# Performance work log

Hardware: AMD Instinct MI355X
Metric: run time of the kernel (lower is better)

The kernel has to match this reference:

```python
import jax, jax.numpy as jnp
import numpy as np

B, S, D, H = 2, 48, 256, 8
DH = D // H  # depth per head = 32
N = S * S    # flattened pair sequence length = 2304


def setup_inputs() -> dict:
    key = jax.random.key(0)
    ks = jax.random.split(key, 9)
    std = 1.0 / np.sqrt(D)
    x = jax.random.normal(ks[0], (B, S, S, D), dtype=jnp.float32)
    Wq = jax.random.normal(ks[1], (D, D), dtype=jnp.float32) * std
    Wk = jax.random.normal(ks[2], (D, D), dtype=jnp.float32) * std
    Wv = jax.random.normal(ks[3], (D, D), dtype=jnp.float32) * std
    Wo = jax.random.normal(ks[4], (D, D), dtype=jnp.float32) * std
    bq = jnp.zeros((D,), jnp.float32)
    bk = jnp.zeros((D,), jnp.float32)
    bv = jnp.zeros((D,), jnp.float32)
    bo = jnp.zeros((D,), jnp.float32)
    return {"pair_representation": x, "Wq": Wq, "bq": bq, "Wk": Wk, "bk": bk,
            "Wv": Wv, "bv": bv, "Wo": Wo, "bo": bo}


def reference(pair_representation, Wq, bq, Wk, bk, Wv, bv, Wo, bo):
    x = pair_representation.reshape(B, N, D)  # flatten (S,S) -> N

    def heads(t):  # (B,N,D) -> (B,H,N,DH)
        return t.reshape(B, N, H, DH).transpose(0, 2, 1, 3)

    q = heads(x @ Wq + bq)
    k = heads(x @ Wk + bk)
    v = heads(x @ Wv + bv)

    scale = 1.0 / jnp.sqrt(jnp.asarray(DH, jnp.float32))
    logits = jnp.einsum('bhnd,bhmd->bhnm', q, k) * scale  # (B,H,N,N)
    attn = jax.nn.softmax(logits, axis=-1)
    ctx = jnp.einsum('bhnm,bhmd->bhnd', attn, v)
    ctx = ctx.transpose(0, 2, 1, 3).reshape(B, N, D)
    return ctx @ Wo + bo  # (B, N, D)
```

## Files before the change

### kernel.cpp

```cpp
#include <hip/hip_runtime.h>
#include <math.h>

#define B 2
#define S 48
#define D 256
#define H 8
#define DH 32
#define N (S*S)
#define BN (B*N)
#define BH (B*H)
#define KS 6
#define KPZ (N/KS)
#define NE ((size_t)BN*D)
#define BHN (BH*N)

typedef _Float16 half8 __attribute__((ext_vector_type(8)));
typedef _Float16 half4_t __attribute__((ext_vector_type(4)));
typedef unsigned short ushort8_t __attribute__((ext_vector_type(8)));
typedef float floatx4 __attribute__((ext_vector_type(4)));

__device__ __forceinline__ half8 cvt8(const float* v) {
    half8 h;
    #pragma unroll
    for (int j = 0; j < 8; j++) h[j] = (_Float16)v[j];
    return h;
}

__global__ __launch_bounds__(256) void proj_kernel(
    const float* __restrict__ x,
    const float* __restrict__ Wq, const float* __restrict__ bq,
    const float* __restrict__ Wk, const float* __restrict__ bk,
    const float* __restrict__ Wv, const float* __restrict__ bv,
    _Float16* __restrict__ qbuf, _Float16* __restrict__ kbuf,
    _Float16* __restrict__ vtbuf)
{
    __shared__ __align__(16) _Float16 BhS[128 * 72];

    const int z = blockIdx.z;
    const float* W    = (z == 0) ? Wq : (z == 1) ? Wk : Wv;
    const float* bias = (z == 0) ? bq : (z == 1) ? bk : bv;
    const float scale = (z == 0) ? rsqrtf((float)DH) * 1.44269504f : 1.0f;

    const int t = threadIdx.x;
    const int wv2 = t >> 6, lane = t & 63, l15 = lane & 15, quad = lane >> 4;
    const int rowb = blockIdx.x * 64;
    const int colb = blockIdx.y * 128;
    const int grow = rowb + wv2 * 16 + l15;
    floatx4 acc[8] = {{0,0,0,0},{0,0,0,0},{0,0,0,0},{0,0,0,0},
                      {0,0,0,0},{0,0,0,0},{0,0,0,0},{0,0,0,0}};

    for (int kb0 = 0; kb0 < D; kb0 += 64) {
        __syncthreads();
        #pragma unroll
        for (int i = 0; i < 4; i++) {
            int u = i * 256 + t;
            int cc = u & 127, k0 = (u >> 7) * 8;
            float v[8];
            #pragma unroll
            for (int j = 0; j < 8; j++)
                v[j] = W[(size_t)(kb0 + k0 + j) * D + colb + cc];
            *(half8*)(BhS + cc * 72 + k0) = cvt8(v);
        }
        __syncthreads();
        #pragma unroll
        for (int ksx = 0; ksx < 2; ksx++) {
            const float* xp = x + (size_t)grow * D + kb0 + ksx * 32 + quad * 8;
            float4 x0 = *(const float4*)xp;
            float4 x1 = *(const float4*)(xp + 4);
            float v[8] = {x0.x, x0.y, x0.z, x0.w, x1.x, x1.y, x1.z, x1.w};
            half8 ah = cvt8(v);
            #pragma unroll
            for (int cg = 0; cg < 8; cg++) {
                half8 bh8 = *(const half8*)(BhS + (cg * 16 + l15) * 72 + ksx * 32 + quad * 8);
                acc[cg] = __builtin_amdgcn_mfma_f32_16x16x32_f16(ah, bh8, acc[cg], 0, 0, 0);
            }
        }
    }

    const int bb = (rowb >= N) ? 1 : 0;
    #pragma unroll
    for (int cg = 0; cg < 8; cg++) {
        int col = colb + cg * 16 + l15;
        int hh = col >> 5, dh = col & 31;
        float bs = bias[col];
        if (z < 2) {
            _Float16* op = (z == 0) ? qbuf : kbuf;
            #pragma unroll
            for (int r = 0; r < 4; r++) {
                int n = rowb + wv2 * 16 + quad * 4 + r - bb * N;
                float v = (acc[cg][r] + bs) * scale;
                op[((size_t)(bb * H + hh) * N + n) * DH + dh] = (_Float16)v;
            }
        } else {
            int n0 = rowb + wv2 * 16 + quad * 4 - bb * N;
            half4_t pk;
            #pragma unroll
            for (int r = 0; r < 4; r++) pk[r] = (_Float16)(acc[cg][r] + bs);
            *(half4_t*)(vtbuf + ((size_t)(bb * H + hh) * DH + dh) * N + n0) = pk;
        }
    }
}

__global__ __launch_bounds__(256) void attn_kernel(
    const _Float16* __restrict__ qbuf, const _Float16* __restrict__ kbuf,
    const _Float16* __restrict__ vtbuf,
    _Float16* __restrict__ ctx_part, float* __restrict__ lpart)
{
    __shared__ __align__(16) _Float16 Ks[128 * 40];
    __shared__ __align__(16) _Float16 Vt[32 * 136];

    const int t = threadIdx.x;
    const int wv2 = t >> 6, lane = t & 63, l15 = lane & 15, quad = lane >> 4;
    const int bh = blockIdx.y, kz = blockIdx.z;
    const int qbase = blockIdx.x * 128 + wv2 * 32;

    half8 bq8[2];
    #pragma unroll
    for (int qg = 0; qg < 2; qg++)
        bq8[qg] = *(const half8*)(qbuf +
            ((size_t)bh * N + qbase + qg * 16 + l15) * DH + quad * 8);

    floatx4 acc[2][2] = {{{0,0,0,0},{0,0,0,0}},{{0,0,0,0},{0,0,0,0}}};
    float lsum[2] = {0.f, 0.f};

    for (int it = 0; it < KPZ / 128; it++) {
        const int key0 = kz * KPZ + it * 128;
        __syncthreads();
        #pragma unroll
        for (int i = 0; i < 2; i++) {
            int u = i * 256 + t;
            *(ushort8_t*)(Ks + (u >> 2) * 40 + (u & 3) * 8) =
                *(const ushort8_t*)(kbuf + ((size_t)bh * N + key0 + (u >> 2)) * DH + (u & 3) * 8);
            *(ushort8_t*)(Vt + (u >> 4) * 136 + (u & 15) * 8) =
                *(const ushort8_t*)(vtbuf + ((size_t)bh * DH + (u >> 4)) * N + key0 + (u & 15) * 8);
        }
        __syncthreads();

        #pragma unroll
        for (int kg = 0; kg < 8; kg++) {
            half8 ka = *(const half8*)(Ks + (kg * 16 + l15) * 40 + quad * 8);
            half4_t va0 = *(const half4_t*)(Vt + l15 * 136 + kg * 16 + quad * 4);
            half4_t va1 = *(const half4_t*)(Vt + (16 + l15) * 136 + kg * 16 + quad * 4);
            #pragma unroll
            for (int qg = 0; qg < 2; qg++) {
                floatx4 s = {0, 0, 0, 0};
                s = __builtin_amdgcn_mfma_f32_16x16x32_f16(ka, bq8[qg], s, 0, 0, 0);
                half4_t pf;
                #pragma unroll
                for (int r = 0; r < 4; r++) {
                    float p = exp2f(s[r]);
                    lsum[qg] += p;
                    pf[r] = (_Float16)p;
                }
                acc[qg][0] = __builtin_amdgcn_mfma_f32_16x16x16f16(va0, pf, acc[qg][0], 0, 0, 0);
                acc[qg][1] = __builtin_amdgcn_mfma_f32_16x16x16f16(va1, pf, acc[qg][1], 0, 0, 0);
            }
        }
    }

    const int bb = bh >> 3, hh = bh & 7;
    #pragma unroll
    for (int qg = 0; qg < 2; qg++) {
        float ls = lsum[qg];
        ls += __shfl_xor(ls, 16);
        ls += __shfl_xor(ls, 32);
        int q = qbase + qg * 16 + l15;
        if (quad == 0) lpart[(size_t)kz * BHN + bh * N + q] = ls;
        _Float16* crow = ctx_part + (size_t)kz * NE + ((size_t)bb * N + q) * D + hh * DH;
        half4_t c0, c1;
        #pragma unroll
        for (int r = 0; r < 4; r++) {
            c0[r] = (_Float16)acc[qg][0][r];
            c1[r] = (_Float16)acc[qg][1][r];
        }
        *(half4_t*)(crow + quad * 4)      = c0;
        *(half4_t*)(crow + 16 + quad * 4) = c1;
    }
}

__global__ __launch_bounds__(256) void outproj_kernel(
    const _Float16* __restrict__ ctx_part, const float* __restrict__ lpart,
    const float* __restrict__ Wo, const float* __restrict__ bo,
    float* __restrict__ out)
{
    __shared__ __align__(16) _Float16 BhS[128 * 72];
    __shared__ __align__(16) _Float16 AsS[32 * 72];
    __shared__ float Linv[32 * 8];

    const int t = threadIdx.x;
    const int wv2 = t >> 6, lane = t & 63, l15 = lane & 15, quad = lane >> 4;
    const int wr = wv2 >> 1, wc = wv2 & 1;
    const int rowb = blockIdx.x * 32;
    const int colb = blockIdx.y * 128;

    {
        int r = t >> 3, hh = t & 7;
        int row = rowb + r;
        int bb = (row >= N) ? 1 : 0;
        int bhn = (bb * H + hh) * N + (row - bb * N);
        float ls = 0.f;
        #pragma unroll
        for (int zz = 0; zz < KS; zz++) ls += lpart[(size_t)zz * BHN + bhn];
        Linv[t] = 1.0f / ls;
    }

    floatx4 acc[4] = {{0,0,0,0},{0,0,0,0},{0,0,0,0},{0,0,0,0}};

    for (int kb0 = 0; kb0 < D; kb0 += 64) {
        __syncthreads();
        {
            int r = t >> 3, k0 = (t & 7) * 8;
            int row = rowb + r;
            int kcol = kb0 + k0;
            float linv = Linv[r * 8 + (kcol >> 5)];
            float v[8] = {};
            #pragma unroll
            for (int zz = 0; zz < KS; zz++) {
                half8 h = *(const half8*)(ctx_part + (size_t)zz * NE + (size_t)row * D + kcol);
                #pragma unroll
                for (int j = 0; j < 8; j++) v[j] += (float)h[j];
            }
            #pragma unroll
            for (int j = 0; j < 8; j++) v[j] *= linv;
            *(half8*)(AsS + r * 72 + k0) = cvt8(v);
        }
        #pragma unroll
        for (int i = 0; i < 4; i++) {
            int u = i * 256 + t;
            int cc = u & 127, k0 = (u >> 7) * 8;
            float v[8];
            #pragma unroll
            for (int j = 0; j < 8; j++)
                v[j] = Wo[(size_t)(kb0 + k0 + j) * D + colb + cc];
            *(half8*)(BhS + cc * 72 + k0) = cvt8(v);
        }
        __syncthreads();
        #pragma unroll
        for (int ksx = 0; ksx < 2; ksx++) {
            half8 ah = *(const half8*)(AsS + (wr * 16 + l15) * 72 + ksx * 32 + quad * 8);
            #pragma unroll
            for (int cg = 0; cg < 4; cg++) {
                half8 bh8 = *(const half8*)(BhS + (wc * 64 + cg * 16 + l15) * 72 + ksx * 32 + quad * 8);
                acc[cg] = __builtin_amdgcn_mfma_f32_16x16x32_f16(ah, bh8, acc[cg], 0, 0, 0);
            }
        }
    }

    #pragma unroll
    for (int cg = 0; cg < 4; cg++) {
        int col = colb + wc * 64 + cg * 16 + l15;
        float bs = bo[col];
        #pragma unroll
        for (int r = 0; r < 4; r++) {
            int row = rowb + wr * 16 + quad * 4 + r;
            out[(size_t)row * D + col] = acc[cg][r] + bs;
        }
    }
}

extern "C" void kernel_launch(void* const* d_in, const int* in_sizes, int n_in,
                              void* d_out, int out_size, void* d_ws, size_t ws_size,
                              hipStream_t stream)
{
    const float* x  = (const float*)d_in[0];
    const float* Wq = (const float*)d_in[1];
    const float* bq = (const float*)d_in[2];
    const float* Wk = (const float*)d_in[3];
    const float* bk = (const float*)d_in[4];
    const float* Wv = (const float*)d_in[5];
    const float* bv = (const float*)d_in[6];
    const float* Wo = (const float*)d_in[7];
    const float* bo = (const float*)d_in[8];
    float* out = (float*)d_out;

    _Float16* ctx_part = (_Float16*)d_ws;
    float* lpart    = (float*)(ctx_part + (size_t)KS * NE);
    _Float16* qbuf  = (_Float16*)(lpart + (size_t)KS * BHN);
    _Float16* kbuf  = qbuf + NE;
    _Float16* vtbuf = kbuf + NE;

    proj_kernel<<<dim3(BN / 64, D / 128, 3), 256, 0, stream>>>(
        x, Wq, bq, Wk, bk, Wv, bv, qbuf, kbuf, vtbuf);

    attn_kernel<<<dim3(N / 128, BH, KS), 256, 0, stream>>>(
        qbuf, kbuf, vtbuf, ctx_part, lpart);

    outproj_kernel<<<dim3(BN / 32, D / 128), 256, 0, stream>>>(
        ctx_part, lpart, Wo, bo, out);
}
```

Measured before the change: 132.0 us.

## Pre-convert x and weights to fp16 in a prep kernel; restructure outproj tiling

Adds a prep kernel that converts x to fp16 and transposes all four weight matrices into fp16 column-major once. The projection and output kernels then load fp16 data with vector loads instead of doing strided fp32 gathers and conversions. The output projection reads Wo straight from global memory with smaller 16-row tiles. The attention kernel packs probabilities with cvt_pkrtz and stores the partial row sums in a per-row layout so outproj can read them contiguously. The cost is an extra launch plus an extra write and read of x in fp16.

Result: no change. 132.3 us (+0.2%).

```diff
diff --git a/kernel.cpp b/kernel.cpp
--- a/kernel.cpp
+++ b/kernel.cpp
@@ -16,6 +16,7 @@
 
 typedef _Float16 half8 __attribute__((ext_vector_type(8)));
 typedef _Float16 half4_t __attribute__((ext_vector_type(4)));
+typedef __fp16 fp16x2 __attribute__((ext_vector_type(2)));
 typedef unsigned short ushort8_t __attribute__((ext_vector_type(8)));
 typedef float floatx4 __attribute__((ext_vector_type(4)));
 
@@ -26,18 +27,57 @@
     return h;
 }
 
+__global__ __launch_bounds__(256) void prep_kernel(
+    const float* __restrict__ x,
+    const float* __restrict__ Wq, const float* __restrict__ Wk,
+    const float* __restrict__ Wv, const float* __restrict__ Wo,
+    _Float16* __restrict__ xh, _Float16* __restrict__ Wt)
+{
+    __shared__ __align__(16) _Float16 Ls[64 * 72];
+    const int t = threadIdx.x;
+    const int bid = blockIdx.x;
+    if (bid < 64) {
+        const int z = bid >> 4, tile = bid & 15;
+        const int k0 = (tile >> 2) * 64, c0 = (tile & 3) * 64;
+        const float* W = (z == 0) ? Wq : (z == 1) ? Wk : (z == 2) ? Wv : Wo;
+        #pragma unroll
+        for (int r = 0; r < 4; r++) {
+            int k = r * 16 + (t >> 4);
+            int c = (t & 15) * 4;
+            float4 f = *(const float4*)(W + (size_t)(k0 + k) * D + c0 + c);
+            Ls[(c + 0) * 72 + k] = (_Float16)f.x;
+            Ls[(c + 1) * 72 + k] = (_Float16)f.y;
+            Ls[(c + 2) * 72 + k] = (_Float16)f.z;
+            Ls[(c + 3) * 72 + k] = (_Float16)f.w;
+        }
+        __syncthreads();
+        #pragma unroll
+        for (int i = 0; i < 2; i++) {
+            int u = i * 256 + t;
+            int c = u >> 3, ko = (u & 7) * 8;
+            *(ushort8_t*)(Wt + (size_t)(z * D + c0 + c) * D + k0 + ko) =
+                *(const ushort8_t*)(Ls + c * 72 + ko);
+        }
+    } else {
+        size_t g = ((size_t)(bid - 64) * 256 + t) * 8;
+        float4 f0 = *(const float4*)(x + g);
+        float4 f1 = *(const float4*)(x + g + 4);
+        float v[8] = {f0.x, f0.y, f0.z, f0.w, f1.x, f1.y, f1.z, f1.w};
+        *(half8*)(xh + g) = cvt8(v);
+    }
+}
+
 __global__ __launch_bounds__(256) void proj_kernel(
-    const float* __restrict__ x,
-    const float* __restrict__ Wq, const float* __restrict__ bq,
-    const float* __restrict__ Wk, const float* __restrict__ bk,
-    const float* __restrict__ Wv, const float* __restrict__ bv,
+    const _Float16* __restrict__ xh, const _Float16* __restrict__ Wt,
+    const float* __restrict__ bq, const float* __restrict__ bk,
+    const float* __restrict__ bv,
     _Float16* __restrict__ qbuf, _Float16* __restrict__ kbuf,
     _Float16* __restrict__ vtbuf)
 {
     __shared__ __align__(16) _Float16 BhS[128 * 72];
 
     const int z = blockIdx.z;
-    const float* W    = (z == 0) ? Wq : (z == 1) ? Wk : Wv;
+    const _Float16* Wz = Wt + (size_t)z * D * D;
     const float* bias = (z == 0) ? bq : (z == 1) ? bk : bv;
     const float scale = (z == 0) ? rsqrtf((float)DH) * 1.44269504f : 1.0f;
 
@@ -54,21 +94,14 @@
         #pragma unroll
         for (int i = 0; i < 4; i++) {
             int u = i * 256 + t;
-            int cc = u & 127, k0 = (u >> 7) * 8;
-            float v[8];
-            #pragma unroll
-            for (int j = 0; j < 8; j++)
-                v[j] = W[(size_t)(kb0 + k0 + j) * D + colb + cc];
-            *(half8*)(BhS + cc * 72 + k0) = cvt8(v);
+            int cc = u >> 3, k0 = (u & 7) * 8;
+            *(ushort8_t*)(BhS + cc * 72 + k0) =
+                *(const ushort8_t*)(Wz + (size_t)(colb + cc) * D + kb0 + k0);
         }
         __syncthreads();
         #pragma unroll
         for (int ksx = 0; ksx < 2; ksx++) {
-            const float* xp = x + (size_t)grow * D + kb0 + ksx * 32 + quad * 8;
-            float4 x0 = *(const float4*)xp;
-            float4 x1 = *(const float4*)(xp + 4);
-            float v[8] = {x0.x, x0.y, x0.z, x0.w, x1.x, x1.y, x1.z, x1.w};
-            half8 ah = cvt8(v);
+            half8 ah = *(const half8*)(xh + (size_t)grow * D + kb0 + ksx * 32 + quad * 8);
             #pragma unroll
             for (int cg = 0; cg < 8; cg++) {
                 half8 bh8 = *(const half8*)(BhS + (cg * 16 + l15) * 72 + ksx * 32 + quad * 8);
@@ -145,13 +178,13 @@
             for (int qg = 0; qg < 2; qg++) {
                 floatx4 s = {0, 0, 0, 0};
                 s = __builtin_amdgcn_mfma_f32_16x16x32_f16(ka, bq8[qg], s, 0, 0, 0);
-                half4_t pf;
-                #pragma unroll
-                for (int r = 0; r < 4; r++) {
-                    float p = exp2f(s[r]);
-                    lsum[qg] += p;
-                    pf[r] = (_Float16)p;
-                }
+                float p0 = exp2f(s[0]), p1 = exp2f(s[1]);
+                float p2 = exp2f(s[2]), p3 = exp2f(s[3]);
+                lsum[qg] += (p0 + p1) + (p2 + p3);
+                union { fp16x2 h2[2]; half4_t h4; } pu;
+                pu.h2[0] = __builtin_amdgcn_cvt_pkrtz(p0, p1);
+                pu.h2[1] = __builtin_amdgcn_cvt_pkrtz(p2, p3);
+                half4_t pf = pu.h4;
                 acc[qg][0] = __builtin_amdgcn_mfma_f32_16x16x16f16(va0, pf, acc[qg][0], 0, 0, 0);
                 acc[qg][1] = __builtin_amdgcn_mfma_f32_16x16x16f16(va1, pf, acc[qg][1], 0, 0, 0);
             }
@@ -165,7 +198,8 @@
         ls += __shfl_xor(ls, 16);
         ls += __shfl_xor(ls, 32);
         int q = qbase + qg * 16 + l15;
-        if (quad == 0) lpart[(size_t)kz * BHN + bh * N + q] = ls;
+        if (quad == 0)
+            lpart[((size_t)(bb * N + q) * H + hh) * KS + kz] = ls;
         _Float16* crow = ctx_part + (size_t)kz * NE + ((size_t)bb * N + q) * D + hh * DH;
         half4_t c0, c1;
         #pragma unroll
@@ -180,79 +214,68 @@
 
 __global__ __launch_bounds__(256) void outproj_kernel(
     const _Float16* __restrict__ ctx_part, const float* __restrict__ lpart,
-    const float* __restrict__ Wo, const float* __restrict__ bo,
+    const _Float16* __restrict__ Wot, const float* __restrict__ bo,
     float* __restrict__ out)
 {
-    __shared__ __align__(16) _Float16 BhS[128 * 72];
-    __shared__ __align__(16) _Float16 AsS[32 * 72];
-    __shared__ float Linv[32 * 8];
+    __shared__ __align__(16) _Float16 AsS[16 * 72];
+    __shared__ float Linv[16 * 8];
 
     const int t = threadIdx.x;
     const int wv2 = t >> 6, lane = t & 63, l15 = lane & 15, quad = lane >> 4;
-    const int wr = wv2 >> 1, wc = wv2 & 1;
-    const int rowb = blockIdx.x * 32;
+    const int rowb = blockIdx.x * 16;
     const int colb = blockIdx.y * 128;
 
-    {
+    if (t < 128) {
         int r = t >> 3, hh = t & 7;
         int row = rowb + r;
-        int bb = (row >= N) ? 1 : 0;
-        int bhn = (bb * H + hh) * N + (row - bb * N);
+        const float* lp = lpart + ((size_t)row * H + hh) * KS;
         float ls = 0.f;
         #pragma unroll
-        for (int zz = 0; zz < KS; zz++) ls += lpart[(size_t)zz * BHN + bhn];
+        for (int zz = 0; zz < KS; zz++) ls += lp[zz];
         Linv[t] = 1.0f / ls;
     }
 
-    floatx4 acc[4] = {{0,0,0,0},{0,0,0,0},{0,0,0,0},{0,0,0,0}};
+    floatx4 acc[2] = {{0,0,0,0},{0,0,0,0}};
 
     for (int kb0 = 0; kb0 < D; kb0 += 64) {
         __syncthreads();
         {
-            int r = t >> 3, k0 = (t & 7) * 8;
+            int r = t >> 4, k0 = (t & 15) * 4;
             int row = rowb + r;
             int kcol = kb0 + k0;
             float linv = Linv[r * 8 + (kcol >> 5)];
-            float v[8] = {};
+            float v[4] = {};
             #pragma unroll
             for (int zz = 0; zz < KS; zz++) {
-                half8 h = *(const half8*)(ctx_part + (size_t)zz * NE + (size_t)row * D + kcol);
+                half4_t h = *(const half4_t*)(ctx_part + (size_t)zz * NE + (size_t)row * D + kcol);
                 #pragma unroll
-                for (int j = 0; j < 8; j++) v[j] += (float)h[j];
-            }
-            #pragma unroll
-            for (int j = 0; j < 8; j++) v[j] *= linv;
-            *(half8*)(AsS + r * 72 + k0) = cvt8(v);
-        }
-        #pragma unroll
-        for (int i = 0; i < 4; i++) {
-            int u = i * 256 + t;
-            int cc = u & 127, k0 = (u >> 7) * 8;
-            float v[8];
-            #pragma unroll
-            for (int j = 0; j < 8; j++)
-                v[j] = Wo[(size_t)(kb0 + k0 + j) * D + colb + cc];
-            *(half8*)(BhS + cc * 72 + k0) = cvt8(v);
+                for (int j = 0; j < 4; j++) v[j] += (float)h[j];
+            }
+            half4_t hv;
+            #pragma unroll
+            for (int j = 0; j < 4; j++) hv[j] = (_Float16)(v[j] * linv);
+            *(half4_t*)(AsS + r * 72 + k0) = hv;
         }
         __syncthreads();
         #pragma unroll
         for (int ksx = 0; ksx < 2; ksx++) {
-            half8 ah = *(const half8*)(AsS + (wr * 16 + l15) * 72 + ksx * 32 + quad * 8);
-            #pragma unroll
-            for (int cg = 0; cg < 4; cg++) {
-                half8 bh8 = *(const half8*)(BhS + (wc * 64 + cg * 16 + l15) * 72 + ksx * 32 + quad * 8);
+            half8 ah = *(const half8*)(AsS + l15 * 72 + ksx * 32 + quad * 8);
+            #pragma unroll
+            for (int cg = 0; cg < 2; cg++) {
+                half8 bh8 = *(const half8*)(Wot +
+                    (size_t)(colb + wv2 * 32 + cg * 16 + l15) * D + kb0 + ksx * 32 + quad * 8);
                 acc[cg] = __builtin_amdgcn_mfma_f32_16x16x32_f16(ah, bh8, acc[cg], 0, 0, 0);
             }
         }
     }
 
     #pragma unroll
-    for (int cg = 0; cg < 4; cg++) {
-        int col = colb + wc * 64 + cg * 16 + l15;
+    for (int cg = 0; cg < 2; cg++) {
+        int col = colb + wv2 * 32 + cg * 16 + l15;
         float bs = bo[col];
         #pragma unroll
         for (int r = 0; r < 4; r++) {
-            int row = rowb + wr * 16 + quad * 4 + r;
+            int row = rowb + quad * 4 + r;
             out[(size_t)row * D + col] = acc[cg][r] + bs;
         }
     }
@@ -278,13 +301,18 @@
     _Float16* qbuf  = (_Float16*)(lpart + (size_t)KS * BHN);
     _Float16* kbuf  = qbuf + NE;
     _Float16* vtbuf = kbuf + NE;
+    _Float16* xh    = vtbuf + NE;
+    _Float16* Wt    = xh + NE;
+
+    prep_kernel<<<dim3(64 + (int)(NE / 2048)), 256, 0, stream>>>(
+        x, Wq, Wk, Wv, Wo, xh, Wt);
 
     proj_kernel<<<dim3(BN / 64, D / 128, 3), 256, 0, stream>>>(
-        x, Wq, bq, Wk, bk, Wv, bv, qbuf, kbuf, vtbuf);
+        xh, Wt, bq, bk, bv, qbuf, kbuf, vtbuf);
 
     attn_kernel<<<dim3(N / 128, BH, KS), 256, 0, stream>>>(
         qbuf, kbuf, vtbuf, ctx_part, lpart);
 
-    outproj_kernel<<<dim3(BN / 32, D / 128), 256, 0, stream>>>(
-        ctx_part, lpart, Wo, bo, out);
-}
+    outproj_kernel<<<dim3(BN / 16, D / 128), 256, 0, stream>>>(
+        ctx_part, lpart, Wt + 3 * (size_t)D * D, bo, out);
+}
```
